# Optimization experiments

Hardware: AMD Instinct MI355X
Metric: run time of the kernel (lower is better)

## Reference

```python
import jax, jax.numpy as jnp
import numpy as np

B, T, U = 4, 448, 448
SKS, BKS, H, V = 96, 32, 96, 128


def setup_inputs() -> dict:
    key = jax.random.key(0)
    ks = jax.random.split(key, 8)
    return {
        "s": jax.random.normal(ks[0], (B, T, SKS), jnp.float32),
        "b": jax.random.normal(ks[1], (B, U, BKS), jnp.float32),
        "W_sh": jax.random.normal(ks[2], (H, SKS), jnp.float32) * (1.0 / np.sqrt(SKS)),
        "b_sh": jax.random.normal(ks[3], (H,), jnp.float32) * 0.02,
        "W_bh": jax.random.normal(ks[4], (H, BKS), jnp.float32) * (1.0 / np.sqrt(BKS)),
        "b_bh": jax.random.normal(ks[5], (H,), jnp.float32) * 0.02,
        "W_out": jax.random.normal(ks[6], (V, H), jnp.float32) * (1.0 / np.sqrt(H)),
        "b_out": jax.random.normal(ks[7], (V,), jnp.float32) * 0.02,
    }


def reference(s, b, W_sh, b_sh, W_bh, b_bh, W_out, b_out):
    # input projections (self.sh / self.bh): [B,T,H] and [B,U,H]
    sh = jnp.einsum("bts,hs->bth", s, W_sh) + b_sh
    bh = jnp.einsum("buk,hk->buh", b, W_bh) + b_bh
    # broadcast outer-expand + relu gate: z[b,t,u,h] = sh[b,t,h] * relu(bh[b,u,h])
    z = sh[:, :, None, :] * jax.nn.relu(bh)[:, None, :, :]  # [B,T,U,H]
    # output projection (self.out) + log_softmax over vocab
    logits = jnp.einsum("btuh,vh->btuv", z, W_out) + b_out  # [B,T,U,V]
    return jax.nn.log_softmax(logits, axis=-1)
```

## Files before the change

### kernel.cpp

```cpp
#include <hip/hip_runtime.h>

#define B_ 4
#define T_ 448
#define U_ 448
#define SKS_ 96
#define BKS_ 32
#define H_ 96
#define V_ 128

typedef __attribute__((ext_vector_type(8))) short bf16x8;
typedef __attribute__((ext_vector_type(4))) float f32x4;
typedef __attribute__((ext_vector_type(4))) int i32x4;

__device__ __forceinline__ unsigned short f2bf(float f) {
    unsigned int u = __float_as_uint(f);
    u += 0x7fffu + ((u >> 16) & 1u);
    return (unsigned short)(u >> 16);
}
__device__ __forceinline__ float bf2f(unsigned short h) {
    return __uint_as_float(((unsigned int)h) << 16);
}

__global__ __launch_bounds__(128) void prep_kernel(
    const float* __restrict__ s, const float* __restrict__ b,
    const float* __restrict__ W_sh, const float* __restrict__ b_sh,
    const float* __restrict__ W_bh, const float* __restrict__ b_bh,
    const float* __restrict__ W_out,
    unsigned short* __restrict__ sh_ws,
    unsigned short* __restrict__ rbh_ws,
    unsigned short* __restrict__ w_ws)
{
    const int blk = blockIdx.x;
    const int tid = threadIdx.x;

    if (blk < B_ * T_) {
        __shared__ float row[SKS_];
        if (tid < SKS_) row[tid] = s[(size_t)blk * SKS_ + tid];
        __syncthreads();
        if (tid < H_) {
            const float* w = W_sh + (size_t)tid * SKS_;
            float acc = b_sh[tid];
            #pragma unroll
            for (int k = 0; k < SKS_; k += 4) {
                acc += row[k] * w[k] + row[k + 1] * w[k + 1]
                     + row[k + 2] * w[k + 2] + row[k + 3] * w[k + 3];
            }
            sh_ws[(size_t)blk * H_ + tid] = f2bf(acc);
        }
    } else if (blk < 2 * B_ * T_) {
        const int r = blk - B_ * T_;
        __shared__ float row2[BKS_];
        if (tid < BKS_) row2[tid] = b[(size_t)r * BKS_ + tid];
        __syncthreads();
        if (tid < H_) {
            const float* w = W_bh + (size_t)tid * BKS_;
            float acc = b_bh[tid];
            #pragma unroll
            for (int k = 0; k < BKS_; k += 4) {
                acc += row2[k] * w[k] + row2[k + 1] * w[k + 1]
                     + row2[k + 2] * w[k + 2] + row2[k + 3] * w[k + 3];
            }
            acc = fmaxf(acc, 0.0f);
            rbh_ws[(size_t)r * H_ + tid] = f2bf(acc);
        }
    } else {
        const int c = (blk - 2 * B_ * T_) * 128 + tid;
        const int k8 = c >> 7;
        const int n  = c & 127;
        const float* src = W_out + (size_t)n * H_ + k8 * 8;
        unsigned short tmp[8];
        #pragma unroll
        for (int j = 0; j < 8; j++) tmp[j] = f2bf(src[j]);
        i32x4 v;
        v.x = (int)((unsigned)tmp[0] | ((unsigned)tmp[1] << 16));
        v.y = (int)((unsigned)tmp[2] | ((unsigned)tmp[3] << 16));
        v.z = (int)((unsigned)tmp[4] | ((unsigned)tmp[5] << 16));
        v.w = (int)((unsigned)tmp[6] | ((unsigned)tmp[7] << 16));
        ((i32x4*)w_ws)[c] = v;
    }
}

__global__ __launch_bounds__(256) void joiner_kernel(
    const unsigned short* __restrict__ sh_ws,
    const unsigned short* __restrict__ rbh_ws,
    const unsigned short* __restrict__ w_ws,
    const float* __restrict__ b_out,
    float* __restrict__ out)
{
    __shared__ unsigned short Wl[12 * 128 * 8];
    __shared__ unsigned short Al[12 * 16 * 8];

    const int tid = threadIdx.x;
    const int u0  = blockIdx.x * 16;
    const int t0  = blockIdx.y * 4;
    const int bb  = blockIdx.z;

    {
        const i32x4* src = (const i32x4*)w_ws;
        i32x4* dst = (i32x4*)Wl;
        #pragma unroll
        for (int i = 0; i < 6; i++) {
            const int c = i * 256 + tid;
            dst[c] = src[c];
        }
    }
    if (tid < 192) {
        const int u  = tid & 15;
        const int k8 = tid >> 4;
        const i32x4* src = (const i32x4*)(rbh_ws +
            ((size_t)(bb * U_ + u0 + u)) * H_ + k8 * 8);
        ((i32x4*)Al)[tid] = *src;
    }
    __syncthreads();

    const int wave = tid >> 6;
    const int lane = tid & 63;
    const int t    = t0 + wave;
    const int n    = lane & 15;
    const int q    = lane >> 4;

    const unsigned short* shrow = sh_ws + ((size_t)(bb * T_ + t)) * H_;
    bf16x8 shf[3];
    #pragma unroll
    for (int ks = 0; ks < 3; ks++)
        shf[ks] = *(const bf16x8*)(shrow + ks * 32 + q * 8);

    f32x4 acc[8];
    #pragma unroll
    for (int nt = 0; nt < 8; nt++) acc[nt] = (f32x4){0.f, 0.f, 0.f, 0.f};

    #pragma unroll
    for (int ks = 0; ks < 3; ks++) {
        const bf16x8 rb = *(const bf16x8*)(Al + (ks * 64 + lane) * 8);
        bf16x8 af;
        #pragma unroll
        for (int j = 0; j < 8; j++) {
            const float z = bf2f((unsigned short)shf[ks][j]) *
                            bf2f((unsigned short)rb[j]);
            af[j] = (short)f2bf(z);
        }
        #pragma unroll
        for (int nt = 0; nt < 8; nt++) {
            const bf16x8 wfr = *(const bf16x8*)(Wl +
                ((size_t)((ks * 4 + q) * 128 + nt * 16 + n)) * 8);
            acc[nt] = __builtin_amdgcn_mfma_f32_16x16x32_bf16(wfr, af, acc[nt], 0, 0, 0);
        }
    }

    #pragma unroll
    for (int nt = 0; nt < 8; nt++) {
        const f32x4 bias4 = *(const f32x4*)(b_out + nt * 16 + q * 4);
        acc[nt] += bias4;
    }

    float mx[8];
    #pragma unroll
    for (int nt = 0; nt < 8; nt++)
        mx[nt] = fmaxf(fmaxf(acc[nt][0], acc[nt][1]),
                       fmaxf(acc[nt][2], acc[nt][3]));
    float m = fmaxf(fmaxf(fmaxf(mx[0], mx[1]), fmaxf(mx[2], mx[3])),
                    fmaxf(fmaxf(mx[4], mx[5]), fmaxf(mx[6], mx[7])));
    m = fmaxf(m, __shfl_xor(m, 16, 64));
    m = fmaxf(m, __shfl_xor(m, 32, 64));

    float s0 = 0.f, s1 = 0.f, s2 = 0.f, s3 = 0.f;
    #pragma unroll
    for (int nt = 0; nt < 8; nt++) {
        s0 += __expf(acc[nt][0] - m);
        s1 += __expf(acc[nt][1] - m);
        s2 += __expf(acc[nt][2] - m);
        s3 += __expf(acc[nt][3] - m);
    }
    float ssum = (s0 + s1) + (s2 + s3);
    ssum += __shfl_xor(ssum, 16, 64);
    ssum += __shfl_xor(ssum, 32, 64);

    const float logz = m + __logf(ssum);

    float* orow = out + (((size_t)(bb * T_ + t)) * U_ + (u0 + n)) * V_ + q * 4;
    #pragma unroll
    for (int nt = 0; nt < 8; nt++) {
        f32x4 o = acc[nt] - logz;
        *(f32x4*)(orow + nt * 16) = o;
    }
}

extern "C" void kernel_launch(void* const* d_in, const int* in_sizes, int n_in,
                              void* d_out, int out_size, void* d_ws, size_t ws_size,
                              hipStream_t stream)
{
    const float* s     = (const float*)d_in[0];
    const float* b     = (const float*)d_in[1];
    const float* W_sh  = (const float*)d_in[2];
    const float* b_sh  = (const float*)d_in[3];
    const float* W_bh  = (const float*)d_in[4];
    const float* b_bh  = (const float*)d_in[5];
    const float* W_out = (const float*)d_in[6];
    const float* b_out = (const float*)d_in[7];
    float* out = (float*)d_out;

    unsigned short* sh_ws  = (unsigned short*)d_ws;
    unsigned short* rbh_ws = sh_ws + (size_t)B_ * T_ * H_;
    unsigned short* w_ws   = rbh_ws + (size_t)B_ * U_ * H_;

    prep_kernel<<<2 * B_ * T_ + 12, 128, 0, stream>>>(
        s, b, W_sh, b_sh, W_bh, b_bh, W_out, sh_ws, rbh_ws, w_ws);

    joiner_kernel<<<dim3(U_ / 16, T_ / 4, B_), 256, 0, stream>>>(
        sh_ws, rbh_ws, w_ws, b_out, out);
}
```

Baseline: 439.8 us.

## Process 32 u per block with two MFMA tiles and nontemporal output stores

```diff
diff --git a/kernel.cpp b/kernel.cpp
--- a/kernel.cpp
+++ b/kernel.cpp
@@ -88,10 +88,10 @@
     float* __restrict__ out)
 {
     __shared__ unsigned short Wl[12 * 128 * 8];
-    __shared__ unsigned short Al[12 * 16 * 8];
+    __shared__ unsigned short Al[12 * 32 * 8];
 
     const int tid = threadIdx.x;
-    const int u0  = blockIdx.x * 16;
+    const int u0  = blockIdx.x * 32;
     const int t0  = blockIdx.y * 4;
     const int bb  = blockIdx.z;
 
@@ -104,12 +104,15 @@
             dst[c] = src[c];
         }
     }
-    if (tid < 192) {
-        const int u  = tid & 15;
-        const int k8 = tid >> 4;
-        const i32x4* src = (const i32x4*)(rbh_ws +
-            ((size_t)(bb * U_ + u0 + u)) * H_ + k8 * 8);
-        ((i32x4*)Al)[tid] = *src;
+    {
+        const int c0 = tid;
+        ((i32x4*)Al)[c0] = *(const i32x4*)(rbh_ws +
+            ((size_t)(bb * U_ + u0 + (c0 & 31))) * H_ + (c0 >> 5) * 8);
+        if (tid < 128) {
+            const int c1 = 256 + tid;
+            ((i32x4*)Al)[c1] = *(const i32x4*)(rbh_ws +
+                ((size_t)(bb * U_ + u0 + (c1 & 31))) * H_ + (c1 >> 5) * 8);
+        }
     }
     __syncthreads();
 
@@ -125,63 +128,77 @@
     for (int ks = 0; ks < 3; ks++)
         shf[ks] = *(const bf16x8*)(shrow + ks * 32 + q * 8);
 
-    f32x4 acc[8];
-    #pragma unroll
-    for (int nt = 0; nt < 8; nt++) acc[nt] = (f32x4){0.f, 0.f, 0.f, 0.f};
+    f32x4 acc0[8], acc1[8];
+    #pragma unroll
+    for (int nt = 0; nt < 8; nt++) {
+        acc0[nt] = (f32x4){0.f, 0.f, 0.f, 0.f};
+        acc1[nt] = (f32x4){0.f, 0.f, 0.f, 0.f};
+    }
 
     #pragma unroll
     for (int ks = 0; ks < 3; ks++) {
-        const bf16x8 rb = *(const bf16x8*)(Al + (ks * 64 + lane) * 8);
-        bf16x8 af;
+        const bf16x8 rb0 = *(const bf16x8*)(Al + ((ks * 4 + q) * 32 + n) * 8);
+        const bf16x8 rb1 = *(const bf16x8*)(Al + ((ks * 4 + q) * 32 + 16 + n) * 8);
+        bf16x8 af0, af1;
         #pragma unroll
         for (int j = 0; j < 8; j++) {
-            const float z = bf2f((unsigned short)shf[ks][j]) *
-                            bf2f((unsigned short)rb[j]);
-            af[j] = (short)f2bf(z);
+            const float sv = bf2f((unsigned short)shf[ks][j]);
+            af0[j] = (short)f2bf(sv * bf2f((unsigned short)rb0[j]));
+            af1[j] = (short)f2bf(sv * bf2f((unsigned short)rb1[j]));
         }
         #pragma unroll
         for (int nt = 0; nt < 8; nt++) {
             const bf16x8 wfr = *(const bf16x8*)(Wl +
                 ((size_t)((ks * 4 + q) * 128 + nt * 16 + n)) * 8);
-            acc[nt] = __builtin_amdgcn_mfma_f32_16x16x32_bf16(wfr, af, acc[nt], 0, 0, 0);
-        }
-    }
-
-    #pragma unroll
-    for (int nt = 0; nt < 8; nt++) {
-        const f32x4 bias4 = *(const f32x4*)(b_out + nt * 16 + q * 4);
-        acc[nt] += bias4;
-    }
-
-    float mx[8];
+            acc0[nt] = __builtin_amdgcn_mfma_f32_16x16x32_bf16(wfr, af0, acc0[nt], 0, 0, 0);
+            acc1[nt] = __builtin_amdgcn_mfma_f32_16x16x32_bf16(wfr, af1, acc1[nt], 0, 0, 0);
+        }
+    }
+
+    f32x4 bias4[8];
     #pragma unroll
     for (int nt = 0; nt < 8; nt++)
-        mx[nt] = fmaxf(fmaxf(acc[nt][0], acc[nt][1]),
-                       fmaxf(acc[nt][2], acc[nt][3]));
-    float m = fmaxf(fmaxf(fmaxf(mx[0], mx[1]), fmaxf(mx[2], mx[3])),
-                    fmaxf(fmaxf(mx[4], mx[5]), fmaxf(mx[6], mx[7])));
-    m = fmaxf(m, __shfl_xor(m, 16, 64));
-    m = fmaxf(m, __shfl_xor(m, 32, 64));
-
-    float s0 = 0.f, s1 = 0.f, s2 = 0.f, s3 = 0.f;
-    #pragma unroll
-    for (int nt = 0; nt < 8; nt++) {
-        s0 += __expf(acc[nt][0] - m);
-        s1 += __expf(acc[nt][1] - m);
-        s2 += __expf(acc[nt][2] - m);
-        s3 += __expf(acc[nt][3] - m);
-    }
-    float ssum = (s0 + s1) + (s2 + s3);
-    ssum += __shfl_xor(ssum, 16, 64);
-    ssum += __shfl_xor(ssum, 32, 64);
-
-    const float logz = m + __logf(ssum);
-
-    float* orow = out + (((size_t)(bb * T_ + t)) * U_ + (u0 + n)) * V_ + q * 4;
-    #pragma unroll
-    for (int nt = 0; nt < 8; nt++) {
-        f32x4 o = acc[nt] - logz;
-        *(f32x4*)(orow + nt * 16) = o;
+        bias4[nt] = *(const f32x4*)(b_out + nt * 16 + q * 4);
+
+    const size_t obase = (((size_t)(bb * T_ + t)) * U_ + u0 + n) * V_ + q * 4;
+
+    #pragma unroll
+    for (int half = 0; half < 2; half++) {
+        f32x4* acc = half ? acc1 : acc0;
+
+        #pragma unroll
+        for (int nt = 0; nt < 8; nt++) acc[nt] += bias4[nt];
+
+        float mx[8];
+        #pragma unroll
+        for (int nt = 0; nt < 8; nt++)
+            mx[nt] = fmaxf(fmaxf(acc[nt][0], acc[nt][1]),
+                           fmaxf(acc[nt][2], acc[nt][3]));
+        float m = fmaxf(fmaxf(fmaxf(mx[0], mx[1]), fmaxf(mx[2], mx[3])),
+                        fmaxf(fmaxf(mx[4], mx[5]), fmaxf(mx[6], mx[7])));
+        m = fmaxf(m, __shfl_xor(m, 16, 64));
+        m = fmaxf(m, __shfl_xor(m, 32, 64));
+
+        float s0 = 0.f, s1 = 0.f, s2 = 0.f, s3 = 0.f;
+        #pragma unroll
+        for (int nt = 0; nt < 8; nt++) {
+            s0 += __expf(acc[nt][0] - m);
+            s1 += __expf(acc[nt][1] - m);
+            s2 += __expf(acc[nt][2] - m);
+            s3 += __expf(acc[nt][3] - m);
+        }
+        float ssum = (s0 + s1) + (s2 + s3);
+        ssum += __shfl_xor(ssum, 16, 64);
+        ssum += __shfl_xor(ssum, 32, 64);
+
+        const float logz = m + __logf(ssum);
+
+        float* orow = out + obase + (size_t)half * 16 * V_;
+        #pragma unroll
+        for (int nt = 0; nt < 8; nt++) {
+            f32x4 o = acc[nt] - logz;
+            __builtin_nontemporal_store(o, (f32x4*)(orow + nt * 16));
+        }
     }
 }
 
@@ -206,6 +223,6 @@
     prep_kernel<<<2 * B_ * T_ + 12, 128, 0, stream>>>(
         s, b, W_sh, b_sh, W_bh, b_bh, W_out, sh_ws, rbh_ws, w_ws);
 
-    joiner_kernel<<<dim3(U_ / 16, T_ / 4, B_), 256, 0, stream>>>(
+    joiner_kernel<<<dim3(U_ / 32, T_ / 4, B_), 256, 0, stream>>>(
         sh_ws, rbh_ws, w_ws, b_out, out);
 }
```

Result: slower. 471.2 us (+7.1%).

## Persist joiner blocks over 14 t-tiles with LDS-staged coalesced output stores

Applied to the files above, without the earlier changes.

```diff
diff --git a/kernel.cpp b/kernel.cpp
--- a/kernel.cpp
+++ b/kernel.cpp
@@ -80,20 +80,23 @@
     }
 }
 
-__global__ __launch_bounds__(256) void joiner_kernel(
+__global__ __launch_bounds__(256, 4) void joiner_kernel(
     const unsigned short* __restrict__ sh_ws,
     const unsigned short* __restrict__ rbh_ws,
     const unsigned short* __restrict__ w_ws,
     const float* __restrict__ b_out,
     float* __restrict__ out)
 {
-    __shared__ unsigned short Wl[12 * 128 * 8];
-    __shared__ unsigned short Al[12 * 16 * 8];
-
-    const int tid = threadIdx.x;
-    const int u0  = blockIdx.x * 16;
-    const int t0  = blockIdx.y * 4;
-    const int bb  = blockIdx.z;
+    __shared__ __align__(16) unsigned char SMEM[24576 + 16384];
+    unsigned short* Wl = (unsigned short*)SMEM;
+    f32x4* Ol4 = (f32x4*)(SMEM + 24576);
+
+    const int tid    = threadIdx.x;
+    const int u_tile = blockIdx.x >> 5;
+    const int k      = blockIdx.x & 31;
+    const int bb     = k >> 3;
+    const int tbase  = (k & 7) * 14;
+    const int u0     = u_tile * 16;
 
     {
         const i32x4* src = (const i32x4*)w_ws;
@@ -104,84 +107,118 @@
             dst[c] = src[c];
         }
     }
-    if (tid < 192) {
-        const int u  = tid & 15;
-        const int k8 = tid >> 4;
-        const i32x4* src = (const i32x4*)(rbh_ws +
-            ((size_t)(bb * U_ + u0 + u)) * H_ + k8 * 8);
-        ((i32x4*)Al)[tid] = *src;
-    }
     __syncthreads();
 
     const int wave = tid >> 6;
     const int lane = tid & 63;
-    const int t    = t0 + wave;
     const int n    = lane & 15;
     const int q    = lane >> 4;
 
-    const unsigned short* shrow = sh_ws + ((size_t)(bb * T_ + t)) * H_;
-    bf16x8 shf[3];
+    const unsigned short* rbrow = rbh_ws + ((size_t)(bb * U_ + u0 + n)) * H_;
+    bf16x8 rb[3];
     #pragma unroll
     for (int ks = 0; ks < 3; ks++)
-        shf[ks] = *(const bf16x8*)(shrow + ks * 32 + q * 8);
-
-    f32x4 acc[8];
-    #pragma unroll
-    for (int nt = 0; nt < 8; nt++) acc[nt] = (f32x4){0.f, 0.f, 0.f, 0.f};
-
-    #pragma unroll
-    for (int ks = 0; ks < 3; ks++) {
-        const bf16x8 rb = *(const bf16x8*)(Al + (ks * 64 + lane) * 8);
-        bf16x8 af;
-        #pragma unroll
-        for (int j = 0; j < 8; j++) {
-            const float z = bf2f((unsigned short)shf[ks][j]) *
-                            bf2f((unsigned short)rb[j]);
-            af[j] = (short)f2bf(z);
-        }
+        rb[ks] = *(const bf16x8*)(rbrow + ks * 32 + q * 8);
+
+    f32x4* Olw = Ol4 + wave * 256;
+
+    bf16x8 shf[3];
+    {
+        const int t = (tbase + 0) * 4 + wave;
+        const unsigned short* shrow = sh_ws + ((size_t)(bb * T_ + t)) * H_;
+        #pragma unroll
+        for (int ks = 0; ks < 3; ks++)
+            shf[ks] = *(const bf16x8*)(shrow + ks * 32 + q * 8);
+    }
+
+    #pragma unroll 1
+    for (int i = 0; i < 14; ++i) {
+        const int t = (tbase + i) * 4 + wave;
+
+        f32x4 acc[8];
+        #pragma unroll
+        for (int nt = 0; nt < 8; nt++) acc[nt] = (f32x4){0.f, 0.f, 0.f, 0.f};
+
+        #pragma unroll
+        for (int ks = 0; ks < 3; ks++) {
+            bf16x8 af;
+            #pragma unroll
+            for (int j = 0; j < 8; j++) {
+                const float z = bf2f((unsigned short)shf[ks][j]) *
+                                bf2f((unsigned short)rb[ks][j]);
+                af[j] = (short)f2bf(z);
+            }
+            #pragma unroll
+            for (int nt = 0; nt < 8; nt++) {
+                const bf16x8 wfr = *(const bf16x8*)(Wl +
+                    ((size_t)((ks * 4 + q) * 128 + nt * 16 + n)) * 8);
+                acc[nt] = __builtin_amdgcn_mfma_f32_16x16x32_bf16(wfr, af, acc[nt], 0, 0, 0);
+            }
+        }
+
+        bf16x8 shn[3];
+        {
+            const int inx = (i < 13) ? (i + 1) : i;
+            const int tn  = (tbase + inx) * 4 + wave;
+            const unsigned short* shrow = sh_ws + ((size_t)(bb * T_ + tn)) * H_;
+            #pragma unroll
+            for (int ks = 0; ks < 3; ks++)
+                shn[ks] = *(const bf16x8*)(shrow + ks * 32 + q * 8);
+        }
+
         #pragma unroll
         for (int nt = 0; nt < 8; nt++) {
-            const bf16x8 wfr = *(const bf16x8*)(Wl +
-                ((size_t)((ks * 4 + q) * 128 + nt * 16 + n)) * 8);
-            acc[nt] = __builtin_amdgcn_mfma_f32_16x16x32_bf16(wfr, af, acc[nt], 0, 0, 0);
-        }
-    }
-
-    #pragma unroll
-    for (int nt = 0; nt < 8; nt++) {
-        const f32x4 bias4 = *(const f32x4*)(b_out + nt * 16 + q * 4);
-        acc[nt] += bias4;
-    }
-
-    float mx[8];
-    #pragma unroll
-    for (int nt = 0; nt < 8; nt++)
-        mx[nt] = fmaxf(fmaxf(acc[nt][0], acc[nt][1]),
-                       fmaxf(acc[nt][2], acc[nt][3]));
-    float m = fmaxf(fmaxf(fmaxf(mx[0], mx[1]), fmaxf(mx[2], mx[3])),
-                    fmaxf(fmaxf(mx[4], mx[5]), fmaxf(mx[6], mx[7])));
-    m = fmaxf(m, __shfl_xor(m, 16, 64));
-    m = fmaxf(m, __shfl_xor(m, 32, 64));
-
-    float s0 = 0.f, s1 = 0.f, s2 = 0.f, s3 = 0.f;
-    #pragma unroll
-    for (int nt = 0; nt < 8; nt++) {
-        s0 += __expf(acc[nt][0] - m);
-        s1 += __expf(acc[nt][1] - m);
-        s2 += __expf(acc[nt][2] - m);
-        s3 += __expf(acc[nt][3] - m);
-    }
-    float ssum = (s0 + s1) + (s2 + s3);
-    ssum += __shfl_xor(ssum, 16, 64);
-    ssum += __shfl_xor(ssum, 32, 64);
-
-    const float logz = m + __logf(ssum);
-
-    float* orow = out + (((size_t)(bb * T_ + t)) * U_ + (u0 + n)) * V_ + q * 4;
-    #pragma unroll
-    for (int nt = 0; nt < 8; nt++) {
-        f32x4 o = acc[nt] - logz;
-        *(f32x4*)(orow + nt * 16) = o;
+            const f32x4 bias4 = *(const f32x4*)(b_out + nt * 16 + q * 4);
+            acc[nt] += bias4;
+        }
+
+        float mx[8];
+        #pragma unroll
+        for (int nt = 0; nt < 8; nt++)
+            mx[nt] = fmaxf(fmaxf(acc[nt][0], acc[nt][1]),
+                           fmaxf(acc[nt][2], acc[nt][3]));
+        float m = fmaxf(fmaxf(fmaxf(mx[0], mx[1]), fmaxf(mx[2], mx[3])),
+                        fmaxf(fmaxf(mx[4], mx[5]), fmaxf(mx[6], mx[7])));
+        m = fmaxf(m, __shfl_xor(m, 16, 64));
+        m = fmaxf(m, __shfl_xor(m, 32, 64));
+
+        float s0 = 0.f, s1 = 0.f, s2 = 0.f, s3 = 0.f;
+        #pragma unroll
+        for (int nt = 0; nt < 8; nt++) {
+            s0 += __expf(acc[nt][0] - m);
+            s1 += __expf(acc[nt][1] - m);
+            s2 += __expf(acc[nt][2] - m);
+            s3 += __expf(acc[nt][3] - m);
+        }
+        float ssum = (s0 + s1) + (s2 + s3);
+        ssum += __shfl_xor(ssum, 16, 64);
+        ssum += __shfl_xor(ssum, 32, 64);
+
+        const float logz = m + __logf(ssum);
+
+        const size_t orow0 = (size_t)(bb * T_ + t) * U_ + u0;
+        #pragma unroll
+        for (int p = 0; p < 2; p++) {
+            #pragma unroll
+            for (int w4 = 0; w4 < 4; w4++) {
+                const int nt = p * 4 + w4;
+                const int L  = (n << 4) + (w4 << 2) + q;
+                const int P  = L ^ ((L >> 4) & 7);
+                Olw[P] = acc[nt] - logz;
+            }
+            #pragma unroll
+            for (int ii = 0; ii < 4; ii++) {
+                const int c = (ii << 6) + lane;
+                const int P = c ^ ((c >> 4) & 7);
+                const f32x4 v = Olw[P];
+                const int u = c >> 4;
+                const int j = c & 15;
+                *(f32x4*)(out + (orow0 + u) * V_ + p * 64 + j * 4) = v;
+            }
+        }
+
+        #pragma unroll
+        for (int ks = 0; ks < 3; ks++) shf[ks] = shn[ks];
     }
 }
 
@@ -206,6 +243,6 @@
     prep_kernel<<<2 * B_ * T_ + 12, 128, 0, stream>>>(
         s, b, W_sh, b_sh, W_bh, b_bh, W_out, sh_ws, rbh_ws, w_ws);
 
-    joiner_kernel<<<dim3(U_ / 16, T_ / 4, B_), 256, 0, stream>>>(
+    joiner_kernel<<<dim3(28 * 32), 256, 0, stream>>>(
         sh_ws, rbh_ws, w_ws, b_out, out);
 }
```

After: 601.6 us. 1.37x slower.
